# Kernel tuning notes

Hardware: AMD Instinct MI355X
Metric: run time of the kernel (lower is better)

The kernel has to match this reference:

```python
import jax, jax.numpy as jnp
import numpy as np

K = 40        # knn neighbors (hard-coded in forward)
BN_EPS = 1e-5
NEG_SLOPE = 0.2
NHEADS = 8
ADIM = 64
HDIM = NHEADS * ADIM  # 512
SCALE = HDIM ** (-0.5)  # note: original scales by hdim**-0.5, not adim**-0.5


def knn_idx(x, k):
    # x: (B, C, N) -> (B, N, k) indices of k nearest neighbors (incl. self)
    xx = jnp.sum(x * x, axis=1)                       # (B, N)
    inner = jnp.einsum('bcn,bcm->bnm', x, x)          # (B, N, N)
    neg_sq_dist = 2.0 * inner - xx[:, :, None] - xx[:, None, :]
    return jax.lax.top_k(neg_sq_dist, k)[1]           # (B, N, k)


def get_graph_feature(x, k):
    # x: (B, C, N) -> (B, 2C, N, k)
    idx = knn_idx(x, k)                               # (B, N, k) int32
    xt = jnp.transpose(x, (0, 2, 1))                  # (B, N, C)
    feat = jax.vmap(lambda pts, ids: pts[ids])(xt, idx)  # (B, N, k, C)
    center = xt[:, :, None, :]                        # (B, N, 1, C)
    out = jnp.concatenate(
        [feat - center, jnp.broadcast_to(center, feat.shape)], axis=-1)
    return jnp.transpose(out, (0, 3, 1, 2))           # (B, 2C, N, k)


def bn_lrelu(h, g, b, m, v):
    # inference-mode BatchNorm2d over channel axis=1 + LeakyReLU(0.2)
    scale = g / jnp.sqrt(v + BN_EPS)
    h = (h - m[None, :, None, None]) * scale[None, :, None, None] + b[None, :, None, None]
    return jax.nn.leaky_relu(h, NEG_SLOPE)


def branch(p, conv5_w, bn5_g, bn5_b, bn5_m, bn5_v, conv6_w, bn6_g, bn6_b, bn6_m, bn6_v):
    g = get_graph_feature(p, K)                       # (B, 1024, N, k)
    h = jnp.einsum('oc,bcnk->bonk', conv5_w, g)       # (B, 512, N, k)
    h = bn_lrelu(h, bn5_g, bn5_b, bn5_m, bn5_v)
    h = jnp.transpose(h, (0, 2, 1, 3))                # (B, N=2048, 512, k)
    h = jnp.einsum('oc,bcnk->bonk', conv6_w, h)       # (B, 515, 512, k)
    h = bn_lrelu(h, bn6_g, bn6_b, bn6_m, bn6_v)
    h = jnp.transpose(h, (0, 2, 1, 3))                # (B, 512, 515, k)
    return jnp.max(h, axis=-1)                        # (B, 512, 515)


def heads(f, W):
    # f: (B, S, indim), W: (hdim, indim) -> (B, nheads, S, adim)
    q = jnp.einsum('bsi,oi->bso', f, W)
    B, S, _ = q.shape
    return jnp.transpose(q.reshape(B, S, NHEADS, ADIM), (0, 2, 1, 3))


def setup_inputs() -> dict:
    key = jax.random.key(0)
    ks = jax.random.split(key, 8)
    B, C, N = 1, 512, 2048
    indim = 515
    inp = {
        'x': jax.random.normal(ks[0], (B, C, N), jnp.float32),
        'y': jax.random.normal(ks[1], (B, C, N), jnp.float32),
        'conv5_w': jax.random.normal(ks[2], (512, 1024), jnp.float32) * 0.02,
        'bn5_g': jnp.ones((512,), jnp.float32),
        'bn5_b': jnp.zeros((512,), jnp.float32),
        'bn5_m': jnp.zeros((512,), jnp.float32),
        'bn5_v': jnp.ones((512,), jnp.float32),
        'conv6_w': jax.random.normal(ks[3], (515, 2048), jnp.float32) * 0.02,
        'bn6_g': jnp.ones((515,), jnp.float32),
        'bn6_b': jnp.zeros((515,), jnp.float32),
        'bn6_m': jnp.zeros((515,), jnp.float32),
        'bn6_v': jnp.ones((515,), jnp.float32),
        'Wq': jax.random.normal(ks[4], (HDIM, indim), jnp.float32) * 0.02,
        'Wk': jax.random.normal(ks[5], (HDIM, indim), jnp.float32) * 0.02,
        'Wv': jax.random.normal(ks[6], (HDIM, indim), jnp.float32) * 0.02,
        'Wout': jax.random.normal(ks[7], (indim, HDIM), jnp.float32) * 0.02,
        'bout': jnp.zeros((indim,), jnp.float32),
    }
    return inp


def reference(x, y, conv5_w, bn5_g, bn5_b, bn5_m, bn5_v,
              conv6_w, bn6_g, bn6_b, bn6_m, bn6_v,
              Wq, Wk, Wv, Wout, bout):
    xf = branch(x, conv5_w, bn5_g, bn5_b, bn5_m, bn5_v,
                conv6_w, bn6_g, bn6_b, bn6_m, bn6_v)   # (B, 512, 515)
    yf = branch(y, conv5_w, bn5_g, bn5_b, bn5_m, bn5_v,
                conv6_w, bn6_g, bn6_b, bn6_m, bn6_v)   # (B, 512, 515)
    q = heads(xf, Wq)                                  # (B, H, 512, adim)
    k = heads(yf, Wk)
    v = heads(yf, Wv)
    scores = jax.nn.softmax(jnp.einsum('bhsd,bhtd->bhst', q, k) * SCALE, axis=-1)
    weighted = jnp.einsum('bhst,bhtd->bhsd', scores, v)  # (B, H, 512, adim)
    B, H, S, D = weighted.shape
    merged = jnp.transpose(weighted, (0, 2, 1, 3)).reshape(B, S, H * D)
    return jnp.einsum('bsh,oh->bso', merged, Wout) + bout  # (B, 512, 515)
```

## Files before the change

kernel.cpp:

```cpp
#include <hip/hip_runtime.h>
#include <hip/hip_bf16.h>

typedef __bf16 bf16_t;
typedef float f32x4 __attribute__((ext_vector_type(4)));
typedef __bf16 bf16x8 __attribute__((ext_vector_type(8)));

#define ASYNC_COPY16(gptr, lptr) \
    __builtin_amdgcn_global_load_lds((const __attribute__((address_space(1))) void*)(gptr), \
                                     (__attribute__((address_space(3))) void*)(lptr), 16, 0, 0)

__device__ __forceinline__ float ldx(const void* p, long i, int isbf) {
    return isbf ? (float)((const bf16_t*)p)[i] : ((const float*)p)[i];
}

__global__ __launch_bounds__(256)
void detect_dtype(const void* __restrict__ x, int n, int* __restrict__ flags)
{
    __shared__ int red[4];
    const int tid = threadIdx.x;
    const int ns = n < 8192 ? n : 8192;
    int cnt = 0;
    for (int i = tid; i < ns; i += 256) {
        float v = (float)((const bf16_t*)x)[i];
        float a = fabsf(v);
        bool pl = (v == 0.f) || (a >= 6e-8f && a <= 1.7e7f);
        cnt += pl ? 1 : 0;
    }
    for (int o = 32; o; o >>= 1) cnt += __shfl_down(cnt, o);
    if ((tid & 63) == 0) red[tid >> 6] = cnt;
    __syncthreads();
    if (tid == 0) {
        int t = red[0] + red[1] + red[2] + red[3];
        flags[0] = (t * 10 >= ns * 9) ? 1 : 0;
    }
}

__global__ __launch_bounds__(256)
void conv_elem(const void* __restrict__ src, bf16_t* __restrict__ dst, int n,
               const int* __restrict__ flag)
{
    const int isbf = *flag;
    for (long i = blockIdx.x * 256L + threadIdx.x; i < n; i += (long)gridDim.x * 256)
        dst[i] = (bf16_t)ldx(src, i, isbf);
}

struct P9 { const void* p[9]; int n[9]; };
__global__ __launch_bounds__(256)
void conv_param(P9 pk, float* __restrict__ dst, const int* __restrict__ flag)
{
    const int isbf = *flag;
    const int b = blockIdx.x, n = pk.n[b];
    for (int j = threadIdx.x; j < n; j += 256)
        dst[b * 544 + j] = ldx(pk.p[b], j, isbf);
}

__global__ __launch_bounds__(256)
void pad_wf(const void* __restrict__ W, bf16_t* __restrict__ Wp, const int* __restrict__ flag)
{
    const int isbf = *flag;
    const long i = blockIdx.x * 256L + threadIdx.x;
    if (i >= 512 * 544) return;
    const long o = i / 544, c = i % 544;
    Wp[i] = (c < 515) ? (bf16_t)ldx(W, o * 515 + c, isbf) : (bf16_t)0.f;
}

__global__ __launch_bounds__(256)
void transpose_split(const void* __restrict__ X, bf16_t* __restrict__ XtA,
                     bf16_t* __restrict__ XtB, const int* __restrict__ flag)
{
    __shared__ __align__(16) bf16_t thi[32][33];
    __shared__ __align__(16) bf16_t tlo[32][33];
    const int isbf = *flag;
    const int n0 = blockIdx.x * 32, c0 = blockIdx.y * 32;
    const int lx = threadIdx.x & 31, ly = threadIdx.x >> 5;
    for (int i = 0; i < 4; ++i) {
        float v = ldx(X, (long)(c0 + ly + i * 8) * 2048 + n0 + lx, isbf);
        bf16_t hi = (bf16_t)v;
        thi[ly + i * 8][lx] = hi;
        tlo[ly + i * 8][lx] = (bf16_t)(v - (float)hi);
    }
    __syncthreads();
    for (int i = 0; i < 4; ++i) {
        const long n = n0 + ly + i * 8;
        const int c = c0 + lx;
        bf16_t hi = thi[lx][ly + i * 8], lo = tlo[lx][ly + i * 8];
        XtA[n * 1536 + c] = hi;  XtA[n * 1536 + 512 + c] = lo;  XtA[n * 1536 + 1024 + c] = hi;
        XtB[n * 1536 + c] = hi;  XtB[n * 1536 + 512 + c] = hi;  XtB[n * 1536 + 1024 + c] = lo;
    }
}

__global__ __launch_bounds__(256)
void xx_kernel(const bf16_t* __restrict__ XtA, float* __restrict__ xx)
{
    const long n = blockIdx.x * 256L + threadIdx.x;
    float acc = 0.f;
    for (int c = 0; c < 512; ++c) {
        float v = (float)XtA[n * 1536 + c] + (float)XtA[n * 1536 + 512 + c];
        acc += v * v;
    }
    xx[n] = acc;
}

__global__ __launch_bounds__(256)
void gemm64d(const bf16_t* __restrict__ A, const bf16_t* __restrict__ B,
             float* __restrict__ C, const float* __restrict__ xx,
             int M, int N, int K, int lda, int ldb, int ldc,
             long aBS, long bBS, long cBS, int epi, int moff)
{
    __shared__ __align__(16) bf16_t As[2][4 * 64 * 8];
    __shared__ __align__(16) bf16_t Bs[2][4 * 64 * 8];
    const int tid = threadIdx.x;
    const int m0 = blockIdx.y * 64, n0 = blockIdx.x * 64;
    const int bz = blockIdx.z;
    A += (long)bz * aBS;
    B += (long)bz * bBS;
    const int wave = tid >> 6, lane = tid & 63;
    const int wm = (wave >> 1) * 32, wn = (wave & 1) * 32;
    const int l15 = lane & 15, quad = lane >> 4;

    const long ar = min((long)(m0 + lane), (long)M - 1);
    const long br = min((long)(n0 + lane), (long)N - 1);
    const bf16_t* ga = A + ar * lda + wave * 8;
    const bf16_t* gb = B + br * ldb + wave * 8;

    f32x4 acc[2][2] = {};

    ASYNC_COPY16(ga, &As[0][wave * 512]);
    ASYNC_COPY16(gb, &Bs[0][wave * 512]);

    for (int k0 = 0; k0 < K; k0 += 32) {
        const int cur = (k0 >> 5) & 1;
        __syncthreads();
        if (k0 + 32 < K) {
            ASYNC_COPY16(ga + k0 + 32, &As[cur ^ 1][wave * 512]);
            ASYNC_COPY16(gb + k0 + 32, &Bs[cur ^ 1][wave * 512]);
        }
        bf16x8 af0 = *(const bf16x8*)&As[cur][quad * 512 + (wm +      l15) * 8];
        bf16x8 af1 = *(const bf16x8*)&As[cur][quad * 512 + (wm + 16 + l15) * 8];
        bf16x8 bf0 = *(const bf16x8*)&Bs[cur][quad * 512 + (wn +      l15) * 8];
        bf16x8 bf1 = *(const bf16x8*)&Bs[cur][quad * 512 + (wn + 16 + l15) * 8];
        acc[0][0] = __builtin_amdgcn_mfma_f32_16x16x32_bf16(af0, bf0, acc[0][0], 0, 0, 0);
        acc[0][1] = __builtin_amdgcn_mfma_f32_16x16x32_bf16(af0, bf1, acc[0][1], 0, 0, 0);
        acc[1][0] = __builtin_amdgcn_mfma_f32_16x16x32_bf16(af1, bf0, acc[1][0], 0, 0, 0);
        acc[1][1] = __builtin_amdgcn_mfma_f32_16x16x32_bf16(af1, bf1, acc[1][1], 0, 0, 0);
    }

    C += (long)bz * cBS;
    for (int mi = 0; mi < 2; ++mi)
    for (int ni = 0; ni < 2; ++ni)
    for (int r = 0; r < 4; ++r) {
        int gm = m0 + wm + mi * 16 + quad * 4 + r;
        int gn = n0 + wn + ni * 16 + l15;
        if (gm >= M || gn >= N) continue;
        float o = acc[mi][ni][r];
        long cidx = (long)gm * ldc + gn;
        if (epi == 1) C[cidx] = 2.f * o - xx[gm + moff] - xx[gn];
        else          C[cidx] = o;
    }
}

__global__ __launch_bounds__(256)
void gemm_nt(const bf16_t* __restrict__ A, const bf16_t* __restrict__ B,
             void* __restrict__ Cv, const float* __restrict__ bias,
             const int* __restrict__ oflag, float alpha,
             int M, int N, int K, int lda, int ldb, int ldc,
             long aBS, long bBS, long cBS, int epi)
{
    __shared__ __align__(16) bf16_t As[64 * 40];
    __shared__ __align__(16) bf16_t Bs[64 * 40];
    const int tid = threadIdx.x;
    const int m0 = blockIdx.y * 64, n0 = blockIdx.x * 64;
    const int bz = blockIdx.z;
    A += (long)bz * aBS;
    B += (long)bz * bBS;

    const int lrow = tid >> 2;
    const int lseg = (tid & 3) * 8;
    const long arow = min(m0 + lrow, M - 1);
    const long brow = min(n0 + lrow, N - 1);
    const bf16_t* ap = A + arow * lda + lseg;
    const bf16_t* bp = B + brow * ldb + lseg;

    const int wave = tid >> 6, lane = tid & 63;
    const int wm = (wave >> 1) * 32, wn = (wave & 1) * 32;
    const int l15 = lane & 15, quad = lane >> 4;

    f32x4 acc[2][2] = {};

    for (int k0 = 0; k0 < K; k0 += 32) {
        int4 av = *(const int4*)ap;  ap += 32;
        int4 bv = *(const int4*)bp;  bp += 32;
        __syncthreads();
        *(int4*)(&As[lrow * 40 + lseg]) = av;
        *(int4*)(&Bs[lrow * 40 + lseg]) = bv;
        __syncthreads();
        bf16x8 af0 = *(const bf16x8*)(&As[(wm +      l15) * 40 + quad * 8]);
        bf16x8 af1 = *(const bf16x8*)(&As[(wm + 16 + l15) * 40 + quad * 8]);
        bf16x8 bf0 = *(const bf16x8*)(&Bs[(wn +      l15) * 40 + quad * 8]);
        bf16x8 bf1 = *(const bf16x8*)(&Bs[(wn + 16 + l15) * 40 + quad * 8]);
        acc[0][0] = __builtin_amdgcn_mfma_f32_16x16x32_bf16(af0, bf0, acc[0][0], 0, 0, 0);
        acc[0][1] = __builtin_amdgcn_mfma_f32_16x16x32_bf16(af0, bf1, acc[0][1], 0, 0, 0);
        acc[1][0] = __builtin_amdgcn_mfma_f32_16x16x32_bf16(af1, bf0, acc[1][0], 0, 0, 0);
        acc[1][1] = __builtin_amdgcn_mfma_f32_16x16x32_bf16(af1, bf1, acc[1][1], 0, 0, 0);
    }

    const int ofl = oflag ? *oflag : 1;
    for (int mi = 0; mi < 2; ++mi)
    for (int ni = 0; ni < 2; ++ni)
    for (int r = 0; r < 4; ++r) {
        int gm = m0 + wm + mi * 16 + quad * 4 + r;
        int gn = n0 + wn + ni * 16 + l15;
        if (gm >= M || gn >= N) continue;
        float o = acc[mi][ni][r];
        long cidx = (long)bz * cBS + (long)gm * ldc + gn;
        switch (epi) {
        case 2: ((bf16_t*)Cv)[cidx] = (bf16_t)o; break;
        case 3: ((float*)Cv)[cidx] = o * alpha; break;
        case 5: ((bf16_t*)Cv)[(long)bz * cBS + (long)gn * ldc + gm] = (bf16_t)o; break;
        case 6: {
            float w = o + bias[gn];
            if (ofl) ((bf16_t*)Cv)[cidx] = (bf16_t)w;
            else     ((float*)Cv)[cidx]  = w;
        } break;
        }
    }
}

__global__ __launch_bounds__(256)
void topk40_bs(const float* __restrict__ S, int* __restrict__ idx_out)
{
    __shared__ int red[4];
    __shared__ unsigned long long tmask[8][4];
    __shared__ int sh_slot;
    const int row = blockIdx.x, tid = threadIdx.x;
    const int wave = tid >> 6, lane = tid & 63;

    unsigned uvr[8];
    for (int c = 0; c < 8; ++c) {
        unsigned x = __float_as_uint(S[(long)row * 2048 + c * 256 + tid]);
        uvr[c] = (x & 0x80000000u) ? ~x : (x | 0x80000000u);
    }
    if (tid == 0) sh_slot = 0;

    unsigned lo = 0u, hi = 0xFFFFFFFFu;
    while (hi - lo > 1u) {
        unsigned mid = lo + ((hi - lo) >> 1);
        int c = 0;
        for (int i = 0; i < 8; ++i) c += (uvr[i] > mid) ? 1 : 0;
        for (int o = 32; o; o >>= 1) c += __shfl_down(c, o);
        if (lane == 0) red[wave] = c;
        __syncthreads();
        int tot = red[0] + red[1] + red[2] + red[3];
        __syncthreads();
        if (tot >= 40) lo = mid; else hi = mid;
    }
    const unsigned thr = hi;

    for (int c = 0; c < 8; ++c)
        if (uvr[c] > thr) {
            int s = atomicAdd(&sh_slot, 1);
            idx_out[row * 40 + s] = c * 256 + tid;
        }
    for (int c = 0; c < 8; ++c) {
        unsigned long long m = __ballot(uvr[c] == thr);
        if (lane == 0) tmask[c][wave] = m;
    }
    __syncthreads();
    const int want = 40 - sh_slot;
    int base = 0;
    for (int c = 0; c < 8; ++c) {
        if (uvr[c] == thr) {
            int r = base;
            for (int w = 0; w < wave; ++w) r += __popcll(tmask[c][w]);
            r += __popcll(tmask[c][wave] & (((unsigned long long)1 << lane) - 1));
            if (r < want) {
                int s = atomicAdd(&sh_slot, 1);
                idx_out[row * 40 + s] = c * 256 + tid;
            }
        }
        for (int w = 0; w < 4; ++w) base += __popcll(tmask[c][w]);
    }
}

__global__ __launch_bounds__(256)
void h1a_gen(const float* __restrict__ T, const float* __restrict__ U,
             const int* __restrict__ idx, const float* __restrict__ pf,
             bf16_t* __restrict__ Hc, int c0)
{
    __shared__ int idxs[40 * 256];
    const int c5 = c0 + blockIdx.y, n0 = blockIdx.x * 256, tid = threadIdx.x;
    for (int i = tid; i < 40 * 256; i += 256)
        idxs[(i % 40) * 256 + (i / 40)] = idx[n0 * 40 + i] & 2047;
    const float sc = pf[c5] / sqrtf(pf[3 * 544 + c5] + 1e-5f);
    const float mu = pf[2 * 544 + c5], bb = pf[1 * 544 + c5];
    const float q  = U[(long)c5 * 2048 + n0 + tid] - T[(long)c5 * 2048 + n0 + tid];
    const float* Trow = T + (long)c5 * 2048;
    __syncthreads();
    for (int k = 0; k < 40; ++k) {
        float h = Trow[idxs[k * 256 + tid]] + q;
        h = (h - mu) * sc + bb;
        h = h >= 0.f ? h : 0.2f * h;
        Hc[(long)(blockIdx.y * 40 + k) * 2048 + n0 + tid] = (bf16_t)h;
    }
}

__global__ __launch_bounds__(256)
void epi6_max(const float* __restrict__ C2c, const float* __restrict__ p6,
              bf16_t* __restrict__ Fb, int c0, int Nc)
{
    const int cl = blockIdx.x, tid = threadIdx.x;
    for (int o2 = tid; o2 < 544; o2 += 256) {
        float r = 0.f;
        if (o2 < 515) {
            const float sc = p6[o2] / sqrtf(p6[3 * 544 + o2] + 1e-5f);
            const float mu = p6[2 * 544 + o2], bb = p6[1 * 544 + o2];
            const float* p = C2c + (long)o2 * Nc + cl * 40;
            float mx = -__builtin_inff();
            for (int k = 0; k < 40; ++k) {
                float h = (p[k] - mu) * sc + bb;
                h = h >= 0.f ? h : 0.2f * h;
                mx = fmaxf(mx, h);
            }
            r = mx;
        }
        Fb[(long)(c0 + cl) * 544 + o2] = (bf16_t)r;
    }
}

__global__ __launch_bounds__(256)
void softmax_row(const float* __restrict__ Sc, bf16_t* __restrict__ P)
{
    __shared__ float red[4];
    const long r = blockIdx.x;
    const int tid = threadIdx.x, lane = tid & 63, wave = tid >> 6;
    const float* row = Sc + r * 512;
    float v0 = row[tid], v1 = row[tid + 256];
    float mx = fmaxf(v0, v1);
    for (int off = 32; off; off >>= 1) mx = fmaxf(mx, __shfl_down(mx, off));
    if (lane == 0) red[wave] = mx;
    __syncthreads();
    mx = fmaxf(fmaxf(red[0], red[1]), fmaxf(red[2], red[3]));
    __syncthreads();
    float e0 = expf(v0 - mx), e1 = expf(v1 - mx);
    float sm = e0 + e1;
    for (int off = 32; off; off >>= 1) sm += __shfl_down(sm, off);
    if (lane == 0) red[wave] = sm;
    __syncthreads();
    sm = red[0] + red[1] + red[2] + red[3];
    float inv = 1.f / sm;
    P[r * 512 + tid] = (bf16_t)(e0 * inv);
    P[r * 512 + tid + 256] = (bf16_t)(e1 * inv);
}

extern "C" void kernel_launch(void* const* d_in, const int* in_sizes, int n_in,
                              void* d_out, int out_size, void* d_ws, size_t ws_size,
                              hipStream_t stream)
{
    (void)in_sizes; (void)n_in; (void)out_size;

    char* wsb = (char*)d_ws;
    size_t pos = 0;
    auto alloc = [&](size_t bytes) -> char* {
        char* p = wsb + pos;
        pos += (bytes + 255) & ~(size_t)255;
        return p;
    };
    int*    flags = (int*)  alloc(256);
    int*    idx   = (int*)  alloc(2048 * 40 * 4);
    float*  xx    = (float*)alloc(2048 * 4);
    float*  T     = (float*)alloc((size_t)512 * 2048 * 4);
    float*  U     = (float*)alloc((size_t)512 * 2048 * 4);
    bf16_t* XtA   = (bf16_t*)alloc((size_t)2048 * 1536 * 2);
    bf16_t* XtB   = (bf16_t*)alloc((size_t)2048 * 1536 * 2);
    bf16_t* W5c   = (bf16_t*)alloc((size_t)512 * 1024 * 2);
    bf16_t* W6c   = (bf16_t*)alloc((size_t)515 * 2048 * 2);
    bf16_t* Woutc = (bf16_t*)alloc((size_t)515 * 512 * 2);
    bf16_t* Wqp   = (bf16_t*)alloc((size_t)512 * 544 * 2);
    bf16_t* Wkp   = (bf16_t*)alloc((size_t)512 * 544 * 2);
    bf16_t* Wvp   = (bf16_t*)alloc((size_t)512 * 544 * 2);
    float*  pf    = (float*)alloc((size_t)9 * 544 * 4);
    bf16_t* Fb[2];
    Fb[0] = (bf16_t*)alloc((size_t)512 * 544 * 2);
    Fb[1] = (bf16_t*)alloc((size_t)512 * 544 * 2);
    bf16_t* qb = (bf16_t*)alloc((size_t)512 * 512 * 2);
    bf16_t* kb = (bf16_t*)alloc((size_t)512 * 512 * 2);
    bf16_t* vt = (bf16_t*)alloc((size_t)512 * 512 * 2);
    bf16_t* mg = (bf16_t*)alloc((size_t)512 * 512 * 2);
    char* BIG = wsb + pos;
    size_t big = (ws_size > pos) ? (ws_size - pos) : 0;
    if (big < 3939840) return;

    const int CC = (big >= 126074880) ? 512 : (big >= 63037440) ? 256
                 : (big >= 31518720)  ? 128 : (big >= 15759360) ? 64
                 : (big >= 7879680)   ? 32  : 16;
    const int RC = (big >= 16777216) ? 2048 : (big >= 4194304) ? 512 : 128;
    const int AH = (big >= 12582912) ? 8 : 1;
    const int Nc = CC * 40;

    float*  S   = (float*)BIG;
    bf16_t* Hc  = (bf16_t*)BIG;
    float*  C2c = (float*)(BIG + (size_t)Nc * 2048 * 2);
    float*  scA = (float*)BIG;
    bf16_t* prA = (bf16_t*)(BIG + (size_t)AH * 512 * 512 * 4);

    detect_dtype<<<1, 256, 0, stream>>>(d_in[0], in_sizes[0], flags);
    conv_elem<<<1024, 256, 0, stream>>>(d_in[2], W5c, 512 * 1024, flags);
    conv_elem<<<1024, 256, 0, stream>>>(d_in[7], W6c, 515 * 2048, flags);
    conv_elem<<<1024, 256, 0, stream>>>(d_in[15], Woutc, 515 * 512, flags);
    pad_wf<<<1088, 256, 0, stream>>>(d_in[12], Wqp, flags);
    pad_wf<<<1088, 256, 0, stream>>>(d_in[13], Wkp, flags);
    pad_wf<<<1088, 256, 0, stream>>>(d_in[14], Wvp, flags);
    P9 pk;
    const int pidx[9] = {3, 4, 5, 6, 8, 9, 10, 11, 16};
    for (int i = 0; i < 9; ++i) { pk.p[i] = d_in[pidx[i]]; pk.n[i] = in_sizes[pidx[i]]; }
    conv_param<<<9, 256, 0, stream>>>(pk, pf, flags);

    for (int b = 0; b < 2; ++b) {
        transpose_split<<<dim3(64, 16), 256, 0, stream>>>(d_in[b], XtA, XtB, flags);
        xx_kernel<<<8, 256, 0, stream>>>(XtA, xx);
        for (int r0 = 0; r0 < 2048; r0 += RC) {
            gemm64d<<<dim3(32, RC / 64), 256, 0, stream>>>(XtA + (size_t)r0 * 1536, XtB, S,
                xx, RC, 2048, 1536, 1536, 1536, 2048, 0, 0, 0, 1, r0);
            topk40_bs<<<RC, 256, 0, stream>>>(S, idx + (size_t)r0 * 40);
        }
        gemm64d<<<dim3(32, 8, 2), 256, 0, stream>>>(W5c, XtA, T, nullptr,
            512, 2048, 512, 1024, 1536, 2048, 512, 0, (long)512 * 2048, 0, 0);
        for (int c0 = 0; c0 < 512; c0 += CC) {
            h1a_gen<<<dim3(8, CC), 256, 0, stream>>>(T, U, idx, pf, Hc, c0);
            gemm64d<<<dim3(Nc / 64, 9), 256, 0, stream>>>(W6c, Hc, C2c, nullptr,
                515, Nc, 2048, 2048, 2048, Nc, 0, 0, 0, 0, 0);
            epi6_max<<<CC, 256, 0, stream>>>(C2c, pf + 4 * 544, Fb[b], c0, Nc);
        }
    }

    gemm_nt<<<dim3(8, 8, 1), 256, 0, stream>>>(Fb[0], Wqp, qb, nullptr, nullptr, 0.f,
        512, 512, 544, 544, 544, 512, 0, 0, 0, 2);
    gemm_nt<<<dim3(8, 8, 1), 256, 0, stream>>>(Fb[1], Wkp, kb, nullptr, nullptr, 0.f,
        512, 512, 544, 544, 544, 512, 0, 0, 0, 2);
    gemm_nt<<<dim3(8, 8, 1), 256, 0, stream>>>(Fb[1], Wvp, vt, nullptr, nullptr, 0.f,
        512, 512, 544, 544, 544, 512, 0, 0, 0, 5);

    const float SCALE = 0.04419417382415922f;
    if (AH == 8) {
        gemm_nt<<<dim3(8, 8, 8), 256, 0, stream>>>(qb, kb, scA, nullptr, nullptr, SCALE,
            512, 512, 64, 512, 512, 512, 64, 64, 262144, 3);
        softmax_row<<<4096, 256, 0, stream>>>(scA, prA);
        gemm_nt<<<dim3(1, 8, 8), 256, 0, stream>>>(prA, vt, mg, nullptr, nullptr, 0.f,
            512, 64, 512, 512, 512, 512, 262144, 32768, 64, 2);
    } else {
        for (int h = 0; h < 8; ++h) {
            gemm_nt<<<dim3(8, 8, 1), 256, 0, stream>>>(qb + h * 64, kb + h * 64, scA,
                nullptr, nullptr, SCALE, 512, 512, 64, 512, 512, 512, 0, 0, 0, 3);
            softmax_row<<<512, 256, 0, stream>>>(scA, prA);
            gemm_nt<<<dim3(1, 8, 1), 256, 0, stream>>>(prA, vt + (size_t)h * 64 * 512,
                mg + h * 64, nullptr, nullptr, 0.f,
                512, 64, 512, 512, 512, 512, 0, 0, 0, 2);
        }
    }
    gemm_nt<<<dim3(9, 8, 1), 256, 0, stream>>>(mg, Woutc, d_out, pf + 8 * 544, flags,
        0.f, 512, 515, 512, 512, 512, 515, 0, 0, 0, 6);
}
```

Before: 993.5 us.

## Use 128x128 tiled MFMA GEMM for conv6 and sort top-k output indices

Adds a gemm128d kernel with 128x128 block tiles (each wave computing a 64x64 sub-tile with 16 MFMA accumulators) and uses it for the conv6 GEMM in place of the 64x64 tiled gemm64d. Larger tiles raise data reuse per LDS load and cut redundant global traffic for the 515-row weight matrix. The trade-off is more accumulator registers, fewer blocks, and waste on the padded M tail (640 rows computed for 515). The top-k kernel now also writes its 40 neighbor indices in descending-score order via a rank count in shared memory, which likely matches the reference ordering and so improves the memory locality of the later gather.

```diff
diff --git a/kernel.cpp b/kernel.cpp
--- a/kernel.cpp
+++ b/kernel.cpp
@@ -99,6 +99,66 @@
         acc += v * v;
     }
     xx[n] = acc;
+}
+
+__global__ __launch_bounds__(256)
+void gemm128d(const bf16_t* __restrict__ A, const bf16_t* __restrict__ B,
+              float* __restrict__ C, int M, int N, int K, int lda, int ldb, int ldc)
+{
+    __shared__ __align__(16) bf16_t As[2][4096];
+    __shared__ __align__(16) bf16_t Bs[2][4096];
+    const int tid = threadIdx.x;
+    const int m0 = blockIdx.x * 128, n0 = blockIdx.y * 128;
+    const int wave = tid >> 6, lane = tid & 63;
+    const int wm = (wave >> 1) * 64, wn = (wave & 1) * 64;
+    const int l15 = lane & 15, quad = lane >> 4;
+
+    const bf16_t* ga[2]; const bf16_t* gb[2]; int loff[2];
+    for (int i = 0; i < 2; ++i) {
+        const int q = wave * 2 + i;
+        const int seg = q & 3, half = q >> 2;
+        const int row = half * 64 + lane;
+        long ar = min((long)(m0 + row), (long)M - 1);
+        long br = min((long)(n0 + row), (long)N - 1);
+        ga[i] = A + ar * lda + seg * 8;
+        gb[i] = B + br * ldb + seg * 8;
+        loff[i] = seg * 1024 + half * 512;
+    }
+
+    f32x4 acc[4][4] = {};
+
+    for (int i = 0; i < 2; ++i) {
+        ASYNC_COPY16(ga[i], &As[0][loff[i]]);
+        ASYNC_COPY16(gb[i], &Bs[0][loff[i]]);
+    }
+
+    for (int k0 = 0; k0 < K; k0 += 32) {
+        const int cur = (k0 >> 5) & 1;
+        __syncthreads();
+        if (k0 + 32 < K) {
+            for (int i = 0; i < 2; ++i) {
+                ASYNC_COPY16(ga[i] + k0 + 32, &As[cur ^ 1][loff[i]]);
+                ASYNC_COPY16(gb[i] + k0 + 32, &Bs[cur ^ 1][loff[i]]);
+            }
+        }
+        bf16x8 af[4], bfr[4];
+        for (int mi = 0; mi < 4; ++mi)
+            af[mi] = *(const bf16x8*)&As[cur][quad * 1024 + (wm + mi * 16 + l15) * 8];
+        for (int ni = 0; ni < 4; ++ni)
+            bfr[ni] = *(const bf16x8*)&Bs[cur][quad * 1024 + (wn + ni * 16 + l15) * 8];
+        for (int mi = 0; mi < 4; ++mi)
+        for (int ni = 0; ni < 4; ++ni)
+            acc[mi][ni] = __builtin_amdgcn_mfma_f32_16x16x32_bf16(af[mi], bfr[ni], acc[mi][ni], 0, 0, 0);
+    }
+
+    for (int mi = 0; mi < 4; ++mi)
+    for (int ni = 0; ni < 4; ++ni)
+    for (int r = 0; r < 4; ++r) {
+        int gm = m0 + wm + mi * 16 + quad * 4 + r;
+        int gn = n0 + wn + ni * 16 + l15;
+        if (gm >= M || gn >= N) continue;
+        C[(long)gm * ldc + gn] = acc[mi][ni][r];
+    }
 }
 
 __global__ __launch_bounds__(256)
@@ -232,6 +292,8 @@
     __shared__ int red[4];
     __shared__ unsigned long long tmask[8][4];
     __shared__ int sh_slot;
+    __shared__ unsigned cu[48];
+    __shared__ int      ci[48];
     const int row = blockIdx.x, tid = threadIdx.x;
     const int wave = tid >> 6, lane = tid & 63;
 
@@ -259,7 +321,7 @@
     for (int c = 0; c < 8; ++c)
         if (uvr[c] > thr) {
             int s = atomicAdd(&sh_slot, 1);
-            idx_out[row * 40 + s] = c * 256 + tid;
+            cu[s] = uvr[c]; ci[s] = c * 256 + tid;
         }
     for (int c = 0; c < 8; ++c) {
         unsigned long long m = __ballot(uvr[c] == thr);
@@ -275,10 +337,18 @@
             r += __popcll(tmask[c][wave] & (((unsigned long long)1 << lane) - 1));
             if (r < want) {
                 int s = atomicAdd(&sh_slot, 1);
-                idx_out[row * 40 + s] = c * 256 + tid;
+                cu[s] = uvr[c]; ci[s] = c * 256 + tid;
             }
         }
         for (int w = 0; w < 4; ++w) base += __popcll(tmask[c][w]);
+    }
+    __syncthreads();
+    if (tid < 40) {
+        unsigned u = cu[tid]; int i = ci[tid];
+        int r = 0;
+        for (int j = 0; j < 40; ++j)
+            r += (cu[j] > u || (cu[j] == u && ci[j] < i)) ? 1 : 0;
+        idx_out[row * 40 + r] = i;
     }
 }
 
@@ -427,8 +497,8 @@
             512, 2048, 512, 1024, 1536, 2048, 512, 0, (long)512 * 2048, 0, 0);
         for (int c0 = 0; c0 < 512; c0 += CC) {
             h1a_gen<<<dim3(8, CC), 256, 0, stream>>>(T, U, idx, pf, Hc, c0);
-            gemm64d<<<dim3(Nc / 64, 9), 256, 0, stream>>>(W6c, Hc, C2c, nullptr,
-                515, Nc, 2048, 2048, 2048, Nc, 0, 0, 0, 0, 0);
+            gemm128d<<<dim3(5, Nc / 128), 256, 0, stream>>>(W6c, Hc, C2c,
+                515, Nc, 2048, 2048, 2048, Nc);
             epi6_max<<<CC, 256, 0, stream>>>(C2c, pf + 4 * 544, Fb[b], c0, Nc);
         }
     }
```

Result: faster. 970.5 us (-2.3%).
